# Performance work log

Measured on AMD Instinct MI355X. Metric: run time of the kernel, lower is better.

The kernel has to match this reference:

```python
import jax, jax.numpy as jnp
import numpy as np

B, R, C = 256, 1024, 1024
N_IDX = 64


def setup_inputs() -> dict:
    key = jax.random.key(0)
    kx, = jax.random.split(key, 1)
    x = jax.random.normal(kx, (B, R, C), dtype=jnp.float32)
    rows = jnp.arange(N_IDX, dtype=jnp.int32)
    cols = jnp.arange(N_IDX, dtype=jnp.int32)
    return {"x": x, "rows": rows, "cols": cols}


def _mute_msb(x):
    # frexp: x = m * 2**e with m in [0.5, 1). Muting the MSB of the exponent
    # (per the original: e = 0 if e > 0 else e) multiplies x by 2**(min(e,0)-e),
    # i.e. scales by 2**(-e) when e > 0, identity otherwise.
    e = jnp.frexp(x)[1]                                   # int exponent
    e = jax.lax.stop_gradient(e)
    scale = jnp.where(e > 0, jnp.exp2(-e.astype(x.dtype)), jnp.ones_like(x))
    return x * scale


def reference(x, rows, cols):
    # Boolean mask over the [R, C] plane selecting the (rows x cols) grid.
    mask = jnp.zeros((x.shape[1], x.shape[2]), dtype=bool)
    mask = mask.at[rows[:, None], cols[None, :]].set(True)
    y = _mute_msb(x)
    # Apply only on the selected grid, broadcast over batch.
    return jnp.where(mask[None, :, :], y, x)
```

## Files before the change

### kernel.cpp

```cpp
#include <hip/hip_runtime.h>
#include <hip/hip_bf16.h>


#define RR 1024
#define CC 1024

__global__ void build_masks_kernel(const int* __restrict__ rows,
                                   const int* __restrict__ cols,
                                   unsigned* __restrict__ masks,
                                   int nr, int nc) {
    int t = threadIdx.x;
    if (t < 64) masks[t] = 0u;
    __syncthreads();
    if (t < nr) {
        int r = rows[t];
        atomicOr(&masks[r >> 5], 1u << (r & 31));
    }
    if (t < nc) {
        int c = cols[t];
        atomicOr(&masks[32 + (c >> 5)], 1u << (c & 31));
    }
}

__global__ void copy_mute_kernel(const float4* __restrict__ x,
                                 float4* __restrict__ out,
                                 const unsigned* __restrict__ masks,
                                 long long nq) {
    long long stride = (long long)gridDim.x * blockDim.x;
    for (long long q = (long long)blockIdx.x * blockDim.x + threadIdx.x;
         q < nq; q += stride) {
        float4 v = x[q];
        int r = (int)((q >> 8) & 1023);
        unsigned rowbit  = (masks[r >> 5] >> (r & 31)) & 1u;
        unsigned colword = masks[32 + (int)((q >> 3) & 31)];
        unsigned colbits = (colword >> (((int)q & 7) * 4)) & 0xFu;
        unsigned m = rowbit ? colbits : 0u;
        if (m) {
            float* f = reinterpret_cast<float*>(&v);
#pragma unroll
            for (int k = 0; k < 4; ++k) {
                if ((m >> k) & 1u) {
                    unsigned u = __float_as_uint(f[k]);
                    unsigned E = (u >> 23) & 0xffu;
                    if (E >= 127u && E < 255u)
                        f[k] = __uint_as_float((u & 0x807fffffu) | (126u << 23));
                }
            }
        }
        out[q] = v;
    }
}

extern "C" void kernel_launch(void* const* d_in, const int* in_sizes, int n_in,
                              void* d_out, int out_size, void* d_ws, size_t ws_size,
                              hipStream_t stream) {
    const float* x  = (const float*)d_in[0];
    const int* rows = (const int*)d_in[1];
    const int* cols = (const int*)d_in[2];
    float* out      = (float*)d_out;
    unsigned* masks = (unsigned*)d_ws;

    const int nr = in_sizes[1];
    const int nc = in_sizes[2];

    build_masks_kernel<<<1, 64, 0, stream>>>(rows, cols, masks, nr, nc);

    long long nq = (long long)in_sizes[0] / 4;
    int block = 256;
    int grid = 2048;
    copy_mute_kernel<<<grid, block, 0, stream>>>(
        (const float4*)x, (float4*)out, masks, nq);
}
```

Before: 459.2 us.

## Restructure copy kernel per-row with nontemporal loads/stores and cached masks

Rewrites the streaming copy so each block handles two 1024-float rows per iteration. The row mask is staged in shared memory and the column nibble is computed once per thread. Loads and stores use nontemporal builtins to avoid cache pollution, and the grid doubles to 4096 blocks. It assumes the element count is a multiple of two rows and that each row is exactly 256 float4s.

```diff
diff --git a/kernel.cpp b/kernel.cpp
--- a/kernel.cpp
+++ b/kernel.cpp
@@ -4,6 +4,8 @@
 
 #define RR 1024
 #define CC 1024
+
+typedef float f4 __attribute__((ext_vector_type(4)));
 
 __global__ void build_masks_kernel(const int* __restrict__ rows,
                                    const int* __restrict__ cols,
@@ -22,32 +24,45 @@
     }
 }
 
-__global__ void copy_mute_kernel(const float4* __restrict__ x,
-                                 float4* __restrict__ out,
+__device__ __forceinline__ void mute4(f4& v, unsigned m) {
+#pragma unroll
+    for (int k = 0; k < 4; ++k) {
+        if ((m >> k) & 1u) {
+            unsigned u = __float_as_uint(v[k]);
+            unsigned E = (u >> 23) & 0xffu;
+            if (E >= 127u && E < 255u)
+                v[k] = __uint_as_float((u & 0x807fffffu) | (126u << 23));
+        }
+    }
+}
+
+__global__ void copy_mute_kernel(const f4* __restrict__ x,
+                                 f4* __restrict__ out,
                                  const unsigned* __restrict__ masks,
-                                 long long nq) {
-    long long stride = (long long)gridDim.x * blockDim.x;
-    for (long long q = (long long)blockIdx.x * blockDim.x + threadIdx.x;
-         q < nq; q += stride) {
-        float4 v = x[q];
-        int r = (int)((q >> 8) & 1023);
-        unsigned rowbit  = (masks[r >> 5] >> (r & 31)) & 1u;
-        unsigned colword = masks[32 + (int)((q >> 3) & 31)];
-        unsigned colbits = (colword >> (((int)q & 7) * 4)) & 0xFu;
-        unsigned m = rowbit ? colbits : 0u;
-        if (m) {
-            float* f = reinterpret_cast<float*>(&v);
-#pragma unroll
-            for (int k = 0; k < 4; ++k) {
-                if ((m >> k) & 1u) {
-                    unsigned u = __float_as_uint(f[k]);
-                    unsigned E = (u >> 23) & 0xffu;
-                    if (E >= 127u && E < 255u)
-                        f[k] = __uint_as_float((u & 0x807fffffu) | (126u << 23));
-                }
-            }
-        }
-        out[q] = v;
+                                 int nrows) {
+    __shared__ unsigned rowmask[32];
+    int tid = threadIdx.x;
+    if (tid < 32) rowmask[tid] = masks[tid];
+    __syncthreads();
+
+    unsigned colword = masks[32 + (tid >> 3)];
+    unsigned colnib = (colword >> ((tid & 7) * 4)) & 0xFu;
+
+    for (int row = blockIdx.x * 2; row < nrows; row += gridDim.x * 2) {
+        long long q0 = (long long)row * 256 + tid;
+        f4 v0 = __builtin_nontemporal_load(&x[q0]);
+        f4 v1 = __builtin_nontemporal_load(&x[q0 + 256]);
+
+        int r0 = row & (RR - 1);
+        int r1 = (row + 1) & (RR - 1);
+        unsigned m0 = ((rowmask[r0 >> 5] >> (r0 & 31)) & 1u) ? colnib : 0u;
+        unsigned m1 = ((rowmask[r1 >> 5] >> (r1 & 31)) & 1u) ? colnib : 0u;
+
+        if (m0) mute4(v0, m0);
+        if (m1) mute4(v1, m1);
+
+        __builtin_nontemporal_store(v0, &out[q0]);
+        __builtin_nontemporal_store(v1, &out[q0 + 256]);
     }
 }
 
@@ -65,9 +80,9 @@
 
     build_masks_kernel<<<1, 64, 0, stream>>>(rows, cols, masks, nr, nc);
 
-    long long nq = (long long)in_sizes[0] / 4;
+    int nrows = in_sizes[0] / CC;
     int block = 256;
-    int grid = 2048;
+    int grid = 4096;
     copy_mute_kernel<<<grid, block, 0, stream>>>(
-        (const float4*)x, (float4*)out, masks, nq);
+        (const f4*)x, (f4*)out, masks, nrows);
 }
```

Measured after the change: 399.6 us. -13.0%, faster.
